# Optimization experiments

Measured on AMD Instinct MI355X. Metric: run time of the kernel, lower is better.

The kernel has to match this reference:

```python
import jax, jax.numpy as jnp
import numpy as np

B, S, D, H = 2, 2048, 2048, 32
HD = D // H  # head_dim = 64
NEG = -1e10


def setup_inputs() -> dict:
    key = jax.random.key(0)
    k1, k2, k3 = jax.random.split(key, 3)
    hidden_states = jax.random.normal(k1, (B, S, D), dtype=jnp.float32)
    W = jax.random.normal(k2, (D, 3 * D), dtype=jnp.float32) * (1.0 / np.sqrt(D))
    b = jax.random.normal(k3, (3 * D,), dtype=jnp.float32) * 0.02
    return {"hidden_states": hidden_states, "W": W, "b": b}


def reference(hidden_states, W, b):
    # fused QKV projection: [B,S,D] @ [D,3D] -> [B,S,3D]
    qvk = hidden_states @ W + b
    # OPT interleaved layout: reshape to [B,S,D,3]; channel 0=q, 1=v, 2=k
    qvk = qvk.reshape(B, S, D, 3)
    q = qvk[..., 0].reshape(B, S, H, HD)
    v = qvk[..., 1].reshape(B, S, H, HD)
    k = qvk[..., 2].reshape(B, S, H, HD)
    # causal bias: -1e10 strictly above diagonal, shape [1,1,S,S]
    bias = jnp.triu(jnp.full((S, S), NEG, dtype=jnp.float32), 1)[None, None]
    # dot_product_attention_weights: scale q by 1/sqrt(head_dim)
    scale = jnp.asarray(1.0 / np.sqrt(HD), dtype=jnp.float32)
    scores = jnp.einsum('bqhd,bkhd->bhqk', q * scale, k) + bias  # [B,H,S,S]
    attn_weights = jax.nn.softmax(scores, axis=-1)
    attn_output = jnp.einsum('bhqk,bkhd->bqhd', attn_weights, v)  # [B,S,H,HD]
    return attn_output.reshape(B, S, D)
```

## Files before the change

### kernel.cpp

```cpp
#include <hip/hip_runtime.h>
#include <hip/hip_bf16.h>
#include <stdint.h>

typedef unsigned short ushort_t;
typedef __bf16 bf16x8 __attribute__((ext_vector_type(8)));
typedef float f32x4 __attribute__((ext_vector_type(4)));
typedef float f32x16 __attribute__((ext_vector_type(16)));
typedef int int4v __attribute__((ext_vector_type(4)));
typedef ushort_t ushort8 __attribute__((ext_vector_type(8)));

__device__ __forceinline__ ushort_t f2bf(float f) {
  union { float f; unsigned int u; } v; v.f = f;
  unsigned int r = v.u + 0x7fffu + ((v.u >> 16) & 1u);
  return (ushort_t)(r >> 16);
}

__device__ __forceinline__ bf16x8 ld_bf8(const ushort_t* p) {
  return *reinterpret_cast<const bf16x8*>(p);
}

__device__ __forceinline__ void g2lds16(const void* g, void* l) {
  __builtin_amdgcn_global_load_lds(
      (const __attribute__((address_space(1))) unsigned int*)g,
      (__attribute__((address_space(3))) unsigned int*)l,
      16, 0, 0);
}

__device__ __forceinline__ float ex2(float x) { return __builtin_amdgcn_exp2f(x); }

__device__ __forceinline__ int cvtpk(float a, float b) {
  int r;
  asm("v_cvt_pk_bf16_f32 %0, %1, %2" : "=v"(r) : "v"(a), "v"(b));
  return r;
}

__global__ __launch_bounds__(256) void cvt_hs(const float* __restrict__ in,
                                              ushort_t* __restrict__ out) {
  int i = (blockIdx.x * 256 + threadIdx.x) * 8;
  float4 a = *reinterpret_cast<const float4*>(in + i);
  float4 b = *reinterpret_cast<const float4*>(in + i + 4);
  ushort8 r;
  r[0] = f2bf(a.x); r[1] = f2bf(a.y); r[2] = f2bf(a.z); r[3] = f2bf(a.w);
  r[4] = f2bf(b.x); r[5] = f2bf(b.y); r[6] = f2bf(b.z); r[7] = f2bf(b.w);
  *reinterpret_cast<ushort8*>(out + i) = r;
}

__global__ __launch_bounds__(256) void transpose_W(const float* __restrict__ Win,
                                                   ushort_t* __restrict__ Wt) {
  __shared__ ushort_t T[64][65];
  const int t = threadIdx.x;
  const int k0 = (blockIdx.x & 31) * 64;
  const int n0 = (blockIdx.x >> 5) * 64;
#pragma unroll
  for (int i = 0; i < 16; ++i) {
    int idx = i * 256 + t;
    int r = idx >> 6, c = idx & 63;
    T[r][c] = f2bf(Win[(k0 + r) * 6144 + n0 + c]);
  }
  __syncthreads();
#pragma unroll
  for (int i = 0; i < 16; ++i) {
    int idx = i * 256 + t;
    int nr = idx >> 6, kc = idx & 63;
    Wt[(n0 + nr) * 2048 + k0 + kc] = T[kc][nr];
  }
}

__global__ __launch_bounds__(256, 2) void gemm_qkv(
    const ushort_t* __restrict__ A, const ushort_t* __restrict__ Bt,
    const float* __restrict__ bias,
    ushort_t* __restrict__ Qb, ushort_t* __restrict__ Kb,
    ushort_t* __restrict__ VT) {
  __shared__ __align__(16) char smem[40960];
  ushort_t* A0 = (ushort_t*)smem;
  ushort_t* A1 = (ushort_t*)(smem + 8192);
  ushort_t* B0 = (ushort_t*)(smem + 16384);
  ushort_t* B1 = (ushort_t*)(smem + 28672);
  ushort_t* Cs = (ushort_t*)smem;
  const int t = threadIdx.x;
  const int w = t >> 6, l = t & 63;
  const int lo = l & 15, hi = l >> 4;
  const int wr = w >> 1, wc = w & 1;

  int bid = blockIdx.x;
  int swz = (bid & 7) * 128 + (bid >> 3);
  const int mt = swz & 31, nt = swz >> 5;
  const int bm = mt * 128;
  const int bn = nt * 192;

  f32x4 acc[4][6];
#pragma unroll
  for (int i = 0; i < 4; ++i)
#pragma unroll
    for (int j = 0; j < 6; ++j) acc[i][j] = f32x4{0.f, 0.f, 0.f, 0.f};

  const ushort_t* Ag = A + (size_t)bm * 2048;
  const ushort_t* Bg = Bt + (size_t)bn * 2048;

#define STAGE(Ad, Bd, kk_)                                       \
  do {                                                           \
    for (int r2 = 0; r2 < 2; ++r2) {                             \
      int c_ = r2 * 256 + t;                                     \
      int row_ = c_ >> 2, s4_ = c_ & 3;                          \
      int slot_ = s4_ ^ ((row_ & 3) ^ ((row_ >> 2) & 3));        \
      g2lds16(Ag + row_ * 2048 + (kk_) + slot_ * 8, (Ad) + c_ * 8); \
    }                                                            \
    for (int r3 = 0; r3 < 3; ++r3) {                             \
      int c_ = r3 * 256 + t;                                     \
      int row_ = c_ >> 2, s4_ = c_ & 3;                          \
      int slot_ = s4_ ^ ((row_ & 3) ^ ((row_ >> 2) & 3));        \
      g2lds16(Bg + row_ * 2048 + (kk_) + slot_ * 8, (Bd) + c_ * 8); \
    }                                                            \
  } while (0)

  STAGE(A0, B0, 0);
  __syncthreads();
  ushort_t *Ac = A0, *Bc = B0, *An = A1, *Bn = B1;

  for (int kk = 0; kk < 2048; kk += 32) {
    if (kk + 32 < 2048) STAGE(An, Bn, kk + 32);
    bf16x8 af[4], bfr[6];
#pragma unroll
    for (int mf = 0; mf < 4; ++mf) {
      int row = wr * 64 + mf * 16 + lo;
      int fr = (row & 3) ^ ((row >> 2) & 3);
      af[mf] = ld_bf8(Ac + row * 32 + ((hi ^ fr) << 3));
    }
#pragma unroll
    for (int nf = 0; nf < 6; ++nf) {
      int row = wc * 96 + nf * 16 + lo;
      int fr = (row & 3) ^ ((row >> 2) & 3);
      bfr[nf] = ld_bf8(Bc + row * 32 + ((hi ^ fr) << 3));
    }
    __builtin_amdgcn_s_setprio(1);
#pragma unroll
    for (int mf = 0; mf < 4; ++mf)
#pragma unroll
      for (int nf = 0; nf < 6; ++nf)
        acc[mf][nf] = __builtin_amdgcn_mfma_f32_16x16x32_bf16(
            af[mf], bfr[nf], acc[mf][nf], 0, 0, 0);
    __builtin_amdgcn_s_setprio(0);
    __syncthreads();
    ushort_t* tmp;
    tmp = Ac; Ac = An; An = tmp;
    tmp = Bc; Bc = Bn; Bn = tmp;
  }
#undef STAGE

  float bv[6];
  int ch[6];
#pragma unroll
  for (int nf = 0; nf < 6; ++nf) {
    int nl = wc * 96 + nf * 16 + lo;
    bv[nf] = bias[bn + nl];
    ch[nf] = nl % 3;
  }
  const int b_ = bm >> 11;
  const int bh = (b_ << 5) + nt;
  const float QS = 0.125f * 1.44269504f;

#pragma unroll
  for (int h = 0; h < 2; ++h) {
    if (wr == h) {
#pragma unroll
      for (int mf = 0; mf < 4; ++mf)
#pragma unroll
        for (int nf = 0; nf < 6; ++nf) {
          int rloc = mf * 16 + hi * 4;
          int nl = wc * 96 + nf * 16 + lo;
          f32x4 a = acc[mf][nf];
#pragma unroll
          for (int j = 0; j < 4; ++j) {
            float v = a[j] + bv[nf];
            if (ch[nf] == 0) v *= QS;
            Cs[(rloc + j) * 200 + nl] = f2bf(v);
          }
        }
    }
    __syncthreads();
    const int sbase = (bm & 2047) + h * 64;
#pragma unroll
    for (int it = 0; it < 2; ++it) {
      int slot = it * 256 + t;
      int r = slot >> 3, g = slot & 7;
      ushort8 vq, vk;
#pragma unroll
      for (int u = 0; u < 8; ++u) {
        int hd = g * 8 + u;
        vq[u] = Cs[r * 200 + hd * 3];
        vk[u] = Cs[r * 200 + hd * 3 + 2];
      }
      size_t rowoff = ((size_t)bh * 2048 + sbase + r) * 64 + g * 8;
      *reinterpret_cast<ushort8*>(Qb + rowoff) = vq;
      *reinterpret_cast<ushort8*>(Kb + rowoff) = vk;
    }
#pragma unroll
    for (int it = 0; it < 2; ++it) {
      int slot = it * 256 + t;
      int hd = slot >> 3, sg = slot & 7;
      ushort8 vv;
#pragma unroll
      for (int u = 0; u < 8; ++u) vv[u] = Cs[(sg * 8 + u) * 200 + hd * 3 + 1];
      *reinterpret_cast<ushort8*>(VT + ((size_t)bh * 64 + hd) * 2048 + sbase +
                                  sg * 8) = vv;
    }
    __syncthreads();
  }
}

__device__ __forceinline__ void ldkv(const ushort_t* kp, const ushort_t* vp,
                                     bf16x8 k[4], bf16x8 v0[2], bf16x8 v1[2]) {
#pragma unroll
  for (int dc = 0; dc < 4; ++dc) k[dc] = ld_bf8(kp + dc * 16);
#pragma unroll
  for (int s = 0; s < 2; ++s) {
    v0[s] = ld_bf8(vp + s * 16);
    v1[s] = ld_bf8(vp + s * 16 + 32 * 2048);
  }
}

__device__ __forceinline__ void proc_chunk(const bf16x8 kf[4],
                                           const bf16x8 vf0[2],
                                           const bf16x8 vf1[2],
                                           const bf16x8 qf[4], f32x16& o0,
                                           f32x16& o1, float& mr, float& lr,
                                           bool diag, int ql, int hi) {
  f32x16 p;
#pragma unroll
  for (int r = 0; r < 16; ++r) p[r] = 0.f;
  __builtin_amdgcn_s_setprio(1);
#pragma unroll
  for (int dc = 0; dc < 4; ++dc)
    p = __builtin_amdgcn_mfma_f32_32x32x16_bf16(kf[dc], qf[dc], p, 0, 0, 0);
  __builtin_amdgcn_s_setprio(0);
  if (diag) {
#pragma unroll
    for (int r = 0; r < 16; ++r) {
      int kvr = (r & 3) + 8 * (r >> 2) + 4 * hi;
      if (kvr > ql) p[r] = -1e30f;
    }
  }
  float a0 = fmaxf(p[0], p[1]), a1 = fmaxf(p[2], p[3]);
  float a2 = fmaxf(p[4], p[5]), a3 = fmaxf(p[6], p[7]);
  float a4 = fmaxf(p[8], p[9]), a5 = fmaxf(p[10], p[11]);
  float a6 = fmaxf(p[12], p[13]), a7 = fmaxf(p[14], p[15]);
  float mx = fmaxf(fmaxf(fmaxf(a0, a1), fmaxf(a2, a3)),
                   fmaxf(fmaxf(a4, a5), fmaxf(a6, a7)));
  if (__any(mx > mr + 10.0f)) {
    mx = fmaxf(mx, __shfl_xor(mx, 32));
    float mn = fmaxf(mr, mx);
    float scl = ex2(mr - mn);
    mr = mn;
    lr *= scl;
#pragma unroll
    for (int r = 0; r < 16; ++r) { o0[r] *= scl; o1[r] *= scl; }
  }
#pragma unroll
  for (int r = 0; r < 16; ++r) p[r] = ex2(p[r] - mr);
  float s0 = (p[0] + p[1]) + (p[2] + p[3]);
  float s1 = (p[4] + p[5]) + (p[6] + p[7]);
  float s2 = (p[8] + p[9]) + (p[10] + p[11]);
  float s3 = (p[12] + p[13]) + (p[14] + p[15]);
  lr += (s0 + s1) + (s2 + s3);

  __builtin_amdgcn_s_setprio(1);
#pragma unroll
  for (int s = 0; s < 2; ++s) {
    int x0 = cvtpk(p[8 * s + 0], p[8 * s + 1]);
    int x1 = cvtpk(p[8 * s + 2], p[8 * s + 3]);
    int y0 = cvtpk(p[8 * s + 4], p[8 * s + 5]);
    int y1 = cvtpk(p[8 * s + 6], p[8 * s + 7]);
    int ox0 = __shfl_xor(x0, 32);
    int ox1 = __shfl_xor(x1, 32);
    int oy0 = __shfl_xor(y0, 32);
    int oy1 = __shfl_xor(y1, 32);
    int4v wv;
    wv[0] = hi ? oy0 : x0;
    wv[1] = hi ? oy1 : x1;
    wv[2] = hi ? y0 : ox0;
    wv[3] = hi ? y1 : ox1;
    bf16x8 pf = __builtin_bit_cast(bf16x8, wv);
    o0 = __builtin_amdgcn_mfma_f32_32x32x16_bf16(vf0[s], pf, o0, 0, 0, 0);
    o1 = __builtin_amdgcn_mfma_f32_32x32x16_bf16(vf1[s], pf, o1, 0, 0, 0);
  }
  __builtin_amdgcn_s_setprio(0);
}

__global__ __launch_bounds__(64) void attn(
    const ushort_t* __restrict__ Qb, const ushort_t* __restrict__ Kb,
    const ushort_t* __restrict__ VT, float* __restrict__ out) {
  __shared__ float Ld[32 * 66];
  const int l = threadIdx.x;
  const int ql = l & 31, hi = l >> 5;

  const int bid = blockIdx.x;
  const int bh = bid & 63;
  const int p = bid >> 6;
  const int nchB = 64 - p;
  const int q0A = p * 32;
  const int q0B = (63 - p) * 32;
  const int b_ = bh >> 5, h = bh & 31;

  const ushort_t* kbase = Kb + bh * 2048 * 64 + hi * 8;
  const ushort_t* vbase = VT + (bh * 64 + ql) * 2048 + hi * 8;
  const int KSTR = 32 * 64;
  const int VSTR = 32;

  bf16x8 qfA[4], qfB[4];
  {
    const ushort_t* qpA = Qb + (bh * 2048 + q0A + ql) * 64 + hi * 8;
    const ushort_t* qpB = Qb + (bh * 2048 + q0B + ql) * 64 + hi * 8;
#pragma unroll
    for (int dc = 0; dc < 4; ++dc) {
      qfA[dc] = ld_bf8(qpA + dc * 16);
      qfB[dc] = ld_bf8(qpB + dc * 16);
    }
  }

  f32x16 oA0, oA1, oB0, oB1;
#pragma unroll
  for (int r = 0; r < 16; ++r) {
    oA0[r] = 0.f; oA1[r] = 0.f; oB0[r] = 0.f; oB1[r] = 0.f;
  }
  float mA = -1e30f, lA = 0.f, mB = -1e30f, lB = 0.f;

  bf16x8 kX[4], vX0[2], vX1[2], kY[4], vY0[2], vY1[2];
  const ushort_t* kp = kbase + ql * 64;
  const ushort_t* vp = vbase;
  ldkv(kp, vp, kX, vX0, vX1);

  int c = 0;
  while (c + 2 <= nchB) {
    kp += KSTR; vp += VSTR;
    ldkv(kp, vp, kY, vY0, vY1);
    proc_chunk(kX, vX0, vX1, qfB, oB0, oB1, mB, lB, false, ql, hi);
    if (c <= p)
      proc_chunk(kX, vX0, vX1, qfA, oA0, oA1, mA, lA, (c == p), ql, hi);
    if (c + 2 < nchB) {
      kp += KSTR; vp += VSTR;
      ldkv(kp, vp, kX, vX0, vX1);
    }
    proc_chunk(kY, vY0, vY1, qfB, oB0, oB1, mB, lB, (c + 1 == nchB - 1), ql,
               hi);
    if (c + 1 <= p)
      proc_chunk(kY, vY0, vY1, qfA, oA0, oA1, mA, lA, (c + 1 == p), ql, hi);
    c += 2;
  }
  if (c < nchB) {
    proc_chunk(kX, vX0, vX1, qfB, oB0, oB1, mB, lB, true, ql, hi);
    if (c <= p)
      proc_chunk(kX, vX0, vX1, qfA, oA0, oA1, mA, lA, (c == p), ql, hi);
  }

#pragma unroll 1
  for (int tile = 0; tile < 2; ++tile) {
    const float lr = tile ? lB : lA;
    const float lrf = lr + __shfl_xor(lr, 32);
    const float inv = 1.0f / lrf;
    const int q0 = tile ? q0B : q0A;
#pragma unroll
    for (int r = 0; r < 16; ++r) {
      int hdv = (r & 3) + 8 * (r >> 2) + 4 * hi;
      Ld[ql * 66 + hdv] = (tile ? oB0[r] : oA0[r]) * inv;
      Ld[ql * 66 + 32 + hdv] = (tile ? oB1[r] : oA1[r]) * inv;
    }
    __syncthreads();
    float* op = out + (size_t)(b_ * 2048 + q0) * 2048 + h * 64 + l;
#pragma unroll
    for (int i = 0; i < 32; ++i) {
      op[(size_t)i * 2048] = Ld[i * 66 + l];
    }
    __syncthreads();
  }
}

extern "C" void kernel_launch(void* const* d_in, const int* in_sizes, int n_in,
                              void* d_out, int out_size, void* d_ws,
                              size_t ws_size, hipStream_t stream) {
  (void)in_sizes; (void)n_in; (void)out_size; (void)ws_size;
  const float* hs = (const float*)d_in[0];
  const float* W = (const float*)d_in[1];
  const float* bias = (const float*)d_in[2];
  float* out = (float*)d_out;

  char* ws = (char*)d_ws;
  ushort_t* Abf = (ushort_t*)(ws);
  ushort_t* Wt = (ushort_t*)(ws + (16u << 20));
  ushort_t* Qb = (ushort_t*)(ws + (40u << 20));
  ushort_t* Kb = (ushort_t*)(ws + (56u << 20));
  ushort_t* VT = (ushort_t*)(ws + (72u << 20));

  hipLaunchKernelGGL(cvt_hs, dim3(4096), dim3(256), 0, stream, hs, Abf);
  hipLaunchKernelGGL(transpose_W, dim3(3072), dim3(256), 0, stream, W, Wt);
  hipLaunchKernelGGL(gemm_qkv, dim3(1024), dim3(256), 0, stream, Abf, Wt, bias,
                     Qb, Kb, VT);
  hipLaunchKernelGGL(attn, dim3(2048), dim3(64), 0, stream, Qb, Kb, VT, out);
}
```

Baseline: 242.5 us.

## Triple-buffer QKV GEMM LDS staging with explicit vmcnt waits

Turns the QKV projection GEMM's double-buffered global-to-LDS pipeline into a three-stage ring. Loads are issued two K-steps ahead, and partial s_waitcnt vmcnt waits let the newest stage stay in flight while the current one is consumed. The goal is to hide global load latency behind MFMA work. In exchange, LDS use grows from 40KB to 60KB per block, which may limit the 2-blocks-per-CU occupancy, and the loop now has two barriers per iteration.

```diff
diff --git a/kernel.cpp b/kernel.cpp
--- a/kernel.cpp
+++ b/kernel.cpp
@@ -33,6 +33,8 @@
   asm("v_cvt_pk_bf16_f32 %0, %1, %2" : "=v"(r) : "v"(a), "v"(b));
   return r;
 }
+
+#define VMCNT(n) asm volatile("s_waitcnt vmcnt(" #n ")" ::: "memory")
 
 __global__ __launch_bounds__(256) void cvt_hs(const float* __restrict__ in,
                                               ushort_t* __restrict__ out) {
@@ -71,11 +73,11 @@
     const float* __restrict__ bias,
     ushort_t* __restrict__ Qb, ushort_t* __restrict__ Kb,
     ushort_t* __restrict__ VT) {
-  __shared__ __align__(16) char smem[40960];
-  ushort_t* A0 = (ushort_t*)smem;
-  ushort_t* A1 = (ushort_t*)(smem + 8192);
-  ushort_t* B0 = (ushort_t*)(smem + 16384);
-  ushort_t* B1 = (ushort_t*)(smem + 28672);
+  __shared__ __align__(16) char smem[61440];
+  ushort_t* Abuf[3] = {(ushort_t*)smem, (ushort_t*)(smem + 8192),
+                       (ushort_t*)(smem + 16384)};
+  ushort_t* Bbuf[3] = {(ushort_t*)(smem + 24576), (ushort_t*)(smem + 36864),
+                       (ushort_t*)(smem + 49152)};
   ushort_t* Cs = (ushort_t*)smem;
   const int t = threadIdx.x;
   const int w = t >> 6, l = t & 63;
@@ -113,12 +115,15 @@
     }                                                            \
   } while (0)
 
-  STAGE(A0, B0, 0);
-  __syncthreads();
-  ushort_t *Ac = A0, *Bc = B0, *An = A1, *Bn = B1;
-
-  for (int kk = 0; kk < 2048; kk += 32) {
-    if (kk + 32 < 2048) STAGE(An, Bn, kk + 32);
+  ushort_t *Ac = Abuf[0], *An = Abuf[1], *Af = Abuf[2];
+  ushort_t *Bc = Bbuf[0], *Bn = Bbuf[1], *Bf = Bbuf[2];
+
+  STAGE(Ac, Bc, 0);
+  STAGE(An, Bn, 32);
+  VMCNT(5);
+  __builtin_amdgcn_s_barrier();
+
+  for (int tt = 0; tt < 64; ++tt) {
     bf16x8 af[4], bfr[6];
 #pragma unroll
     for (int mf = 0; mf < 4; ++mf) {
@@ -140,10 +145,17 @@
         acc[mf][nf] = __builtin_amdgcn_mfma_f32_16x16x32_bf16(
             af[mf], bfr[nf], acc[mf][nf], 0, 0, 0);
     __builtin_amdgcn_s_setprio(0);
-    __syncthreads();
-    ushort_t* tmp;
-    tmp = Ac; Ac = An; An = tmp;
-    tmp = Bc; Bc = Bn; Bn = tmp;
+    asm volatile("" ::: "memory");
+    __builtin_amdgcn_s_barrier();
+    if (tt + 2 < 64) {
+      STAGE(Af, Bf, (tt + 2) * 32);
+      VMCNT(5);
+    } else {
+      VMCNT(0);
+    }
+    __builtin_amdgcn_s_barrier();
+    ushort_t* ta = Ac; Ac = An; An = Af; Af = ta;
+    ushort_t* tb = Bc; Bc = Bn; Bn = Bf; Bf = tb;
   }
 #undef STAGE
 
```

Result: no change. 244.6 us (+0.9%).
